# Performance work log

Hardware: AMD Instinct MI355X
Metric: run time of the kernel (lower is better)

## Reference

```python
import jax, jax.numpy as jnp
import numpy as np

B, S, D, H, W = 2, 2048, 1024, 16, 16  # batch, seq, embed, heads, window
HD = D // H
DFF = 4 * D
EPS = 1e-5


def _ln(x, g, b):
    m = jnp.mean(x, axis=-1, keepdims=True)
    v = jnp.mean(jnp.square(x - m), axis=-1, keepdims=True)
    return (x - m) * jax.lax.rsqrt(v + EPS) * g + b


def setup_inputs() -> dict:
    key = jax.random.key(0)
    ks = jax.random.split(key, 12)
    s = 0.02
    return {
        "x": jax.random.normal(ks[0], (B, S, D), jnp.float32),
        "ln1_g": jnp.ones((D,), jnp.float32),
        "ln1_b": jnp.zeros((D,), jnp.float32),
        "in_proj_w": jax.random.normal(ks[1], (3 * D, D), jnp.float32) * s,
        "in_proj_b": jnp.zeros((3 * D,), jnp.float32),
        "out_proj_w": jax.random.normal(ks[2], (D, D), jnp.float32) * s,
        "out_proj_b": jnp.zeros((D,), jnp.float32),
        "ln2_g": jnp.ones((D,), jnp.float32),
        "ln2_b": jnp.zeros((D,), jnp.float32),
        "mlp_w1": jax.random.normal(ks[3], (DFF, D), jnp.float32) * s,
        "mlp_b1": jnp.zeros((DFF,), jnp.float32),
        "mlp_w2": jax.random.normal(ks[4], (D, DFF), jnp.float32) * s,
        "mlp_b2": jnp.zeros((D,), jnp.float32),
    }


def reference(x, ln1_g, ln1_b, in_proj_w, in_proj_b, out_proj_w, out_proj_b,
              ln2_g, ln2_b, mlp_w1, mlp_b1, mlp_w2, mlp_b2):
    h = _ln(x, ln1_g, ln1_b)
    qkv = h @ in_proj_w.T + in_proj_b  # [B,S,3D]
    q, k, v = jnp.split(qkv, 3, axis=-1)
    q = q.reshape(B, S, H, HD)
    k = k.reshape(B, S, H, HD)
    v = v.reshape(B, S, H, HD)
    scores = jnp.einsum("bqhd,bkhd->bhqk", q, k) / jnp.sqrt(jnp.float32(HD))
    idx = jnp.arange(S)
    dlt = idx[:, None] - idx[None, :]
    allowed = (dlt >= 0) & (dlt < W)  # causal sliding window, width W
    scores = jnp.where(allowed, scores, -jnp.inf)
    attn = jax.nn.softmax(scores, axis=-1)
    o = jnp.einsum("bhqk,bkhd->bqhd", attn, v).reshape(B, S, D)
    o = o @ out_proj_w.T + out_proj_b
    x = x + o  # residual 1
    xn = _ln(x, ln2_g, ln2_b)
    mlp = jax.nn.gelu(xn @ mlp_w1.T + mlp_b1) @ mlp_w2.T + mlp_b2
    return x + mlp
```

## Files before the change

### kernel.cpp

```cpp
#include <hip/hip_runtime.h>
#include <hip/hip_bf16.h>
#include <cmath>

typedef __bf16 bf16;
typedef __bf16 bf16x4 __attribute__((ext_vector_type(4)));
typedef __bf16 bf16x8 __attribute__((ext_vector_type(8)));
typedef float f32x4 __attribute__((ext_vector_type(4)));

#define BB 2
#define SS 2048
#define DD 1024
#define HH 16
#define WW 16
#define HDD 64
#define DFFD 4096
#define NTOK (BB*SS)

__device__ __forceinline__ float gelu_f(float x) {
    const float k = 1.5957691216057308f;
    float u = k * (x + 0.044715f * x * x * x);
    return x / (1.0f + __expf(-u));
}

__device__ __forceinline__ void glds16(const bf16* g, const bf16* l) {
    __builtin_amdgcn_global_load_lds(
        (const __attribute__((address_space(1))) void*)(uintptr_t)(const void*)g,
        (__attribute__((address_space(3))) void*)(unsigned)(uintptr_t)(const void*)l,
        16, 0, 0);
}

__global__ __launch_bounds__(256) void conv_kernel(
    const float* __restrict__ src, bf16* __restrict__ dst, int n8)
{
    int i = blockIdx.x * 256 + threadIdx.x;
    if (i >= n8) return;
    f32x4 a = *(const f32x4*)(src + (size_t)i * 8);
    f32x4 b = *(const f32x4*)(src + (size_t)i * 8 + 4);
    bf16x8 v;
#pragma unroll
    for (int j = 0; j < 4; j++) { v[j] = (bf16)a[j]; v[4 + j] = (bf16)b[j]; }
    *(bf16x8*)(dst + (size_t)i * 8) = v;
}

__global__ __launch_bounds__(256) void ln_kernel(
    const float* __restrict__ x, const float* __restrict__ g, const float* __restrict__ b,
    bf16* __restrict__ out)
{
    const int row = blockIdx.x, t = threadIdx.x;
    f32x4 v = *(const f32x4*)(x + (size_t)row * DD + t * 4);
    float s  = v[0] + v[1] + v[2] + v[3];
    float s2 = v[0]*v[0] + v[1]*v[1] + v[2]*v[2] + v[3]*v[3];
#pragma unroll
    for (int off = 32; off >= 1; off >>= 1) {
        s  += __shfl_xor(s,  off, 64);
        s2 += __shfl_xor(s2, off, 64);
    }
    __shared__ float red[8];
    const int wave = t >> 6;
    if ((t & 63) == 0) { red[wave] = s; red[4 + wave] = s2; }
    __syncthreads();
    float ts  = red[0] + red[1] + red[2] + red[3];
    float ts2 = red[4] + red[5] + red[6] + red[7];
    float mean = ts * (1.0f / DD);
    float var  = ts2 * (1.0f / DD) - mean * mean;
    float rstd = rsqrtf(var + 1e-5f);
    f32x4 gv = *(const f32x4*)(g + t * 4);
    f32x4 bv = *(const f32x4*)(b + t * 4);
    bf16x4 o;
#pragma unroll
    for (int i = 0; i < 4; i++) o[i] = (bf16)((v[i] - mean) * rstd * gv[i] + bv[i]);
    *(bf16x4*)(out + (size_t)row * DD + t * 4) = o;
}

template<int TM, int ACT, int RESID, int OUTF32>
__global__ __launch_bounds__(256) void gemm_glds(
    const bf16* __restrict__ A, const bf16* __restrict__ Bw,
    const float* __restrict__ bias,
    const float* resid, void* __restrict__ Cout, int N, int K)
{
    constexpr int MI = 4;
    constexpr int NJ = (TM == 128) ? 4 : 2;
    __shared__ __align__(16) bf16 As[2 * TM * 32];
    __shared__ __align__(16) bf16 Bs[2 * 128 * 32];
    const int t = threadIdx.x;
    const int m0 = blockIdx.y * TM, n0 = blockIdx.x * 128;
    const int lane = t & 63, w = t >> 6;
    const int wm = (TM == 128) ? (w & 1) * 64 : 0;
    const int wn = (TM == 128) ? (w >> 1) * 64 : w * 32;
    const int quad = lane >> 4, l16 = lane & 15;
    const int srow = t >> 2, scol = (t & 3) * 8;

    const bf16* Ag = A  + (size_t)(m0 + srow) * K + scol;
    const bf16* Bg = Bw + (size_t)(n0 + srow) * K + scol;

    int k_lo = 0, k_hi = K;
    if (RESID == 3) {
        const int ks = K / gridDim.z;
        k_lo = blockIdx.z * ks;
        k_hi = k_lo + ks;
    }

    auto stage = [&](int buf, int k0) {
        const bf16* AsW = As + buf * (TM * 32) + w * 512;
        const bf16* BsW = Bs + buf * (128 * 32) + w * 512;
        glds16(Ag + k0, AsW);
        if (TM == 128) glds16(Ag + (size_t)64 * K + k0, AsW + 2048);
        glds16(Bg + k0, BsW);
        glds16(Bg + (size_t)64 * K + k0, BsW + 2048);
    };

    const f32x4 zero = {0.f, 0.f, 0.f, 0.f};
    f32x4 acc[MI][NJ];
#pragma unroll
    for (int i = 0; i < MI; i++)
#pragma unroll
        for (int j = 0; j < NJ; j++) acc[i][j] = zero;

    const int nsteps = (k_hi - k_lo) >> 5;
    stage(0, k_lo);
    __syncthreads();

    for (int step = 0; step < nsteps; ++step) {
        const int cur = step & 1;
        if (step + 1 < nsteps)
            stage(cur ^ 1, k_lo + ((step + 1) << 5));
        const bf16* Ab = As + cur * (TM * 32);
        const bf16* Bb = Bs + cur * (128 * 32);
        bf16x8 af[MI], bfr[NJ];
#pragma unroll
        for (int i = 0; i < MI; i++)
            af[i] = *(const bf16x8*)(Ab + (wm + i * 16 + l16) * 32 + quad * 8);
#pragma unroll
        for (int j = 0; j < NJ; j++)
            bfr[j] = *(const bf16x8*)(Bb + (wn + j * 16 + l16) * 32 + quad * 8);
#pragma unroll
        for (int i = 0; i < MI; i++)
#pragma unroll
            for (int j = 0; j < NJ; j++)
                acc[i][j] = __builtin_amdgcn_mfma_f32_16x16x32_bf16(af[i], bfr[j], acc[i][j], 0, 0, 0);
        __syncthreads();
    }

#pragma unroll
    for (int i = 0; i < MI; i++) {
#pragma unroll
        for (int j = 0; j < NJ; j++) {
            int col = n0 + wn + j * 16 + l16;
            float bv = bias[col];
            if (RESID == 3 && blockIdx.z != 0) bv = 0.0f;
#pragma unroll
            for (int r = 0; r < 4; r++) {
                int row = m0 + wm + i * 16 + quad * 4 + r;
                float val = acc[i][j][r] + bv;
                if (ACT == 1) val = gelu_f(val);
                size_t idx = (size_t)row * N + col;
                if (RESID == 2) val += resid[idx];
                if (RESID == 3) {
                    unsafeAtomicAdd(&((float*)Cout)[idx], val);
                } else if (OUTF32) {
                    ((float*)Cout)[idx] = val;
                } else {
                    ((bf16*)Cout)[idx] = (bf16)val;
                }
            }
        }
    }
}

__global__ __launch_bounds__(256) void attn_kernel(
    const bf16* __restrict__ qkv, bf16* __restrict__ o)
{
    __shared__ __align__(16) bf16 Vlds[4][32 * 64];
    __shared__ __align__(16) bf16 Plds[4][16 * 32];
    const int t = threadIdx.x;
    const int w = t >> 6, lane = t & 63;
    const int quad = lane >> 4, l16 = lane & 15;
    const int gw = blockIdx.x * 4 + w;
    const int qb = gw & 127;
    const int h  = (gw >> 7) & (HH - 1);
    const int b  = gw >> 11;
    const int q0 = qb << 4;
    const size_t rs = 3 * DD;
    const bf16* Qb = qkv + (size_t)b * SS * rs + h * HDD;
    const bf16* Kb = Qb + DD;
    const bf16* Vb = Qb + 2 * DD;
    bf16* Vw = Vlds[w];
    bf16* Pw = Plds[w];

    {
        const int sub = lane >> 3;
        const int dc  = (lane & 7) * 8;
#pragma unroll
        for (int c = 0; c < 4; c++) {
            int key = q0 - 16 + c * 8 + sub;
            if (key < 0) key = 0;
            glds16(Vb + (size_t)key * rs + dc, Vw + c * 512);
        }
    }

    const int qrow = q0 + l16;
    int kr0 = q0 - 16 + l16; if (kr0 < 0) kr0 = 0;
    bf16x8 qf0  = *(const bf16x8*)(Qb + (size_t)qrow * rs + quad * 8);
    bf16x8 qf1  = *(const bf16x8*)(Qb + (size_t)qrow * rs + 32 + quad * 8);
    bf16x8 kf0a = *(const bf16x8*)(Kb + (size_t)kr0  * rs + quad * 8);
    bf16x8 kf0b = *(const bf16x8*)(Kb + (size_t)kr0  * rs + 32 + quad * 8);
    bf16x8 kf1a = *(const bf16x8*)(Kb + (size_t)qrow * rs + quad * 8);
    bf16x8 kf1b = *(const bf16x8*)(Kb + (size_t)qrow * rs + 32 + quad * 8);

    const f32x4 zero = {0.f, 0.f, 0.f, 0.f};
    f32x4 acc0 = __builtin_amdgcn_mfma_f32_16x16x32_bf16(qf0, kf0a, zero, 0, 0, 0);
    acc0 = __builtin_amdgcn_mfma_f32_16x16x32_bf16(qf1, kf0b, acc0, 0, 0, 0);
    f32x4 acc1 = __builtin_amdgcn_mfma_f32_16x16x32_bf16(qf0, kf1a, zero, 0, 0, 0);
    acc1 = __builtin_amdgcn_mfma_f32_16x16x32_bf16(qf1, kf1b, acc1, 0, 0, 0);

    float rl[4];
#pragma unroll
    for (int r = 0; r < 4; r++) {
        const int row = quad * 4 + r;
        float s0 = (l16 > row && q0 - 16 + l16 >= 0) ? acc0[r] * 0.125f : -1e30f;
        float s1 = (l16 <= row)                      ? acc1[r] * 0.125f : -1e30f;
        float m = fmaxf(s0, s1);
        m = fmaxf(m, __shfl_xor(m, 1, 64));
        m = fmaxf(m, __shfl_xor(m, 2, 64));
        m = fmaxf(m, __shfl_xor(m, 4, 64));
        m = fmaxf(m, __shfl_xor(m, 8, 64));
        float e0 = __expf(s0 - m), e1 = __expf(s1 - m);
        float sum = e0 + e1;
        sum += __shfl_xor(sum, 1, 64);
        sum += __shfl_xor(sum, 2, 64);
        sum += __shfl_xor(sum, 4, 64);
        sum += __shfl_xor(sum, 8, 64);
        rl[r] = 1.0f / sum;
        Pw[row * 32 + l16]      = (bf16)e0;
        Pw[row * 32 + 16 + l16] = (bf16)e1;
    }

    asm volatile("s_waitcnt vmcnt(0)" ::: "memory");
    bf16x8 pf = *(const bf16x8*)(Pw + l16 * 32 + quad * 8);
#pragma unroll
    for (int dt = 0; dt < 4; dt++) {
        bf16x8 vf;
#pragma unroll
        for (int jj = 0; jj < 8; jj++)
            vf[jj] = Vw[(quad * 8 + jj) * 64 + dt * 16 + l16];
        f32x4 ov = __builtin_amdgcn_mfma_f32_16x16x32_bf16(pf, vf, zero, 0, 0, 0);
#pragma unroll
        for (int r = 0; r < 4; r++) {
            const int row = quad * 4 + r;
            o[(size_t)(b * SS + q0 + row) * DD + h * HDD + dt * 16 + l16] =
                (bf16)(ov[r] * rl[r]);
        }
    }
}

extern "C" void kernel_launch(void* const* d_in, const int* in_sizes, int n_in,
                              void* d_out, int out_size, void* d_ws, size_t ws_size,
                              hipStream_t stream)
{
    (void)in_sizes; (void)n_in; (void)out_size; (void)ws_size;
    const float* x    = (const float*)d_in[0];
    const float* ln1g = (const float*)d_in[1];
    const float* ln1b = (const float*)d_in[2];
    const float* Wqkv = (const float*)d_in[3];
    const float* bqkv = (const float*)d_in[4];
    const float* Wout = (const float*)d_in[5];
    const float* bout = (const float*)d_in[6];
    const float* ln2g = (const float*)d_in[7];
    const float* ln2b = (const float*)d_in[8];
    const float* W1   = (const float*)d_in[9];
    const float* b1   = (const float*)d_in[10];
    const float* W2   = (const float*)d_in[11];
    const float* b2   = (const float*)d_in[12];

    const size_t MB = (size_t)1 << 20;
    char* ws = (char*)d_ws;
    bf16* wqkv_bf = (bf16*)(ws);
    bf16* wout_bf = (bf16*)(ws + 6 * MB);
    bf16* w1_bf   = (bf16*)(ws);
    bf16* w2_bf   = (bf16*)(ws + 8 * MB);
    bf16* qkv     = (bf16*)(ws + 16 * MB);
    bf16* h1      = (bf16*)(ws + 16 * MB);
    bf16* hbuf    = (bf16*)(ws + 48 * MB);
    float* x1     = (float*)d_out;

    const dim3 blk(256);

    conv_kernel<<<(3 * DD * DD / 8) / 256, blk, 0, stream>>>(Wqkv, wqkv_bf, 3 * DD * DD / 8);
    conv_kernel<<<(DD * DD / 8) / 256, blk, 0, stream>>>(Wout, wout_bf, DD * DD / 8);
    ln_kernel<<<NTOK, blk, 0, stream>>>(x, ln1g, ln1b, hbuf);
    gemm_glds<128, 0, 0, 0><<<dim3(24, 32), blk, 0, stream>>>(
        hbuf, wqkv_bf, bqkv, nullptr, qkv, 3 * DD, DD);
    attn_kernel<<<BB * HH * (SS / 16) / 4, blk, 0, stream>>>(qkv, hbuf);
    gemm_glds<64, 0, 2, 1><<<dim3(8, 64), blk, 0, stream>>>(
        hbuf, wout_bf, bout, x, x1, DD, DD);

    conv_kernel<<<(DFFD * DD / 8) / 256, blk, 0, stream>>>(W1, w1_bf, DFFD * DD / 8);
    conv_kernel<<<(DFFD * DD / 8) / 256, blk, 0, stream>>>(W2, w2_bf, DFFD * DD / 8);
    ln_kernel<<<NTOK, blk, 0, stream>>>(x1, ln2g, ln2b, hbuf);
    gemm_glds<128, 1, 0, 0><<<dim3(32, 32), blk, 0, stream>>>(
        hbuf, w1_bf, b1, nullptr, h1, DFFD, DD);
    gemm_glds<128, 0, 3, 1><<<dim3(8, 32, 2), blk, 0, stream>>>(
        h1, w2_bf, b2, nullptr, x1, DD, DFFD);
}
```

Baseline: 316.2 us.

## Add 256x256 eight-wave GEMM with 4-deep LDS ring pipeline for QKV and MLP

Introduces a new GEMM kernel with 512 threads and 256x256 output tiles. It uses a four-stage LDS ring buffer filled by direct global-to-LDS loads, with explicit vmcnt waits and XOR swizzling to avoid bank conflicts, plus block-index swizzling and MFMA priority hints. The QKV, MLP1 and split-K MLP2 GEMMs move to it, and MLP2 now uses 4-way split-K with atomics. The aim is more data reuse per tile and better overlap of loads with MFMA work, at the cost of fewer blocks (low occupancy and wave-quantisation risk) and more atomic traffic.

```diff
diff --git a/kernel.cpp b/kernel.cpp
--- a/kernel.cpp
+++ b/kernel.cpp
@@ -72,6 +72,133 @@
     *(bf16x4*)(out + (size_t)row * DD + t * 4) = o;
 }
 
+template<int ACT, int RESID, int OUTF32>
+__global__ __launch_bounds__(512, 2) void gemm_8p(
+    const bf16* __restrict__ A, const bf16* __restrict__ Bw,
+    const float* __restrict__ bias,
+    void* __restrict__ Cout, int N, int K)
+{
+    __shared__ __align__(16) bf16 ring[4][16384];
+    const int t512 = threadIdx.x;
+    const int lane = t512 & 63, w = t512 >> 6;
+    const int quad = lane >> 4, l16 = lane & 15;
+    const int wm = (w >> 2) * 128;
+    const int wn = (w & 3) * 64;
+
+    const int nb  = gridDim.x * gridDim.y;
+    const int bid = blockIdx.y * gridDim.x + blockIdx.x;
+    const int cpx = nb >> 3;
+    const int swz = (bid & 7) * cpx + (bid >> 3);
+    const int m0 = (swz / gridDim.x) * 256;
+    const int n0 = (swz % gridDim.x) * 256;
+
+    int k_lo = 0, k_hi = K;
+    if (RESID == 3) { const int ks = K / gridDim.z; k_lo = blockIdx.z * ks; k_hi = k_lo + ks; }
+    const int NK = (k_hi - k_lo) >> 5;
+
+    const int srow = t512 >> 2;
+    auto stageA = [&](int u) {
+        const int k0 = k_lo + (u << 5);
+        const bf16* dst = ring[u & 3] + w * 512;
+#pragma unroll
+        for (int ra = 0; ra < 2; ra++) {
+            const int row = ra * 128 + srow;
+            const int q = (t512 & 3) ^ (row & 3);
+            glds16(A + (size_t)(m0 + row) * K + k0 + q * 8, dst + ra * 4096);
+        }
+    };
+    auto stageB = [&](int u) {
+        const int k0 = k_lo + (u << 5);
+        const bf16* dst = ring[u & 3] + 8192 + w * 512;
+#pragma unroll
+        for (int ra = 0; ra < 2; ra++) {
+            const int row = ra * 128 + srow;
+            const int q = (t512 & 3) ^ (row & 3);
+            glds16(Bw + (size_t)(n0 + row) * K + k0 + q * 8, dst + ra * 4096);
+        }
+    };
+
+    const f32x4 zero = {0.f, 0.f, 0.f, 0.f};
+    f32x4 acc[8][4];
+#pragma unroll
+    for (int i = 0; i < 8; i++)
+#pragma unroll
+        for (int j = 0; j < 4; j++) acc[i][j] = zero;
+
+    for (int u = 0; u < 3 && u < NK; ++u) { stageA(u); stageB(u); }
+
+    const int aswz = (l16 & 3);
+    for (int t = 0; t < NK; ++t) {
+        if (t < NK - 2)       asm volatile("s_waitcnt vmcnt(8)" ::: "memory");
+        else if (t == NK - 2) asm volatile("s_waitcnt vmcnt(4)" ::: "memory");
+        else                  asm volatile("s_waitcnt vmcnt(0)" ::: "memory");
+        __builtin_amdgcn_s_barrier();
+        const bf16* Ab = ring[t & 3];
+        const bf16* Bb = Ab + 8192;
+        bf16x8 af[4], bfr[4];
+#pragma unroll
+        for (int i = 0; i < 4; i++) {
+            const int row = wm + i * 16 + l16;
+            af[i] = *(const bf16x8*)(Ab + row * 32 + ((quad ^ aswz) * 8));
+        }
+#pragma unroll
+        for (int j = 0; j < 4; j++) {
+            const int row = wn + j * 16 + l16;
+            bfr[j] = *(const bf16x8*)(Bb + row * 32 + ((quad ^ aswz) * 8));
+        }
+        if (t + 3 < NK) stageA(t + 3);
+        asm volatile("s_waitcnt lgkmcnt(0)" ::: "memory");
+        __builtin_amdgcn_sched_barrier(0);
+        __builtin_amdgcn_s_setprio(1);
+#pragma unroll
+        for (int i = 0; i < 4; i++)
+#pragma unroll
+            for (int j = 0; j < 4; j++)
+                acc[i][j] = __builtin_amdgcn_mfma_f32_16x16x32_bf16(af[i], bfr[j], acc[i][j], 0, 0, 0);
+        __builtin_amdgcn_s_setprio(0);
+        __builtin_amdgcn_s_barrier();
+#pragma unroll
+        for (int i = 0; i < 4; i++) {
+            const int row = wm + 64 + i * 16 + l16;
+            af[i] = *(const bf16x8*)(Ab + row * 32 + ((quad ^ aswz) * 8));
+        }
+        if (t + 3 < NK) stageB(t + 3);
+        asm volatile("s_waitcnt lgkmcnt(0)" ::: "memory");
+        __builtin_amdgcn_sched_barrier(0);
+        __builtin_amdgcn_s_setprio(1);
+#pragma unroll
+        for (int i = 0; i < 4; i++)
+#pragma unroll
+            for (int j = 0; j < 4; j++)
+                acc[4 + i][j] = __builtin_amdgcn_mfma_f32_16x16x32_bf16(af[i], bfr[j], acc[4 + i][j], 0, 0, 0);
+        __builtin_amdgcn_s_setprio(0);
+    }
+
+#pragma unroll
+    for (int i = 0; i < 8; i++) {
+#pragma unroll
+        for (int j = 0; j < 4; j++) {
+            const int col = n0 + wn + j * 16 + l16;
+            float bv = bias[col];
+            if (RESID == 3 && blockIdx.z != 0) bv = 0.0f;
+#pragma unroll
+            for (int r = 0; r < 4; r++) {
+                const int row = m0 + wm + i * 16 + quad * 4 + r;
+                float val = acc[i][j][r] + bv;
+                if (ACT == 1) val = gelu_f(val);
+                size_t idx = (size_t)row * N + col;
+                if (RESID == 3) {
+                    unsafeAtomicAdd(&((float*)Cout)[idx], val);
+                } else if (OUTF32) {
+                    ((float*)Cout)[idx] = val;
+                } else {
+                    ((bf16*)Cout)[idx] = (bf16)val;
+                }
+            }
+        }
+    }
+}
+
 template<int TM, int ACT, int RESID, int OUTF32>
 __global__ __launch_bounds__(256) void gemm_glds(
     const bf16* __restrict__ A, const bf16* __restrict__ Bw,
@@ -93,13 +220,6 @@
     const bf16* Ag = A  + (size_t)(m0 + srow) * K + scol;
     const bf16* Bg = Bw + (size_t)(n0 + srow) * K + scol;
 
-    int k_lo = 0, k_hi = K;
-    if (RESID == 3) {
-        const int ks = K / gridDim.z;
-        k_lo = blockIdx.z * ks;
-        k_hi = k_lo + ks;
-    }
-
     auto stage = [&](int buf, int k0) {
         const bf16* AsW = As + buf * (TM * 32) + w * 512;
         const bf16* BsW = Bs + buf * (128 * 32) + w * 512;
@@ -116,14 +236,14 @@
 #pragma unroll
         for (int j = 0; j < NJ; j++) acc[i][j] = zero;
 
-    const int nsteps = (k_hi - k_lo) >> 5;
-    stage(0, k_lo);
+    const int nsteps = K >> 5;
+    stage(0, 0);
     __syncthreads();
 
     for (int step = 0; step < nsteps; ++step) {
         const int cur = step & 1;
         if (step + 1 < nsteps)
-            stage(cur ^ 1, k_lo + ((step + 1) << 5));
+            stage(cur ^ 1, (step + 1) << 5);
         const bf16* Ab = As + cur * (TM * 32);
         const bf16* Bb = Bs + cur * (128 * 32);
         bf16x8 af[MI], bfr[NJ];
@@ -147,7 +267,6 @@
         for (int j = 0; j < NJ; j++) {
             int col = n0 + wn + j * 16 + l16;
             float bv = bias[col];
-            if (RESID == 3 && blockIdx.z != 0) bv = 0.0f;
 #pragma unroll
             for (int r = 0; r < 4; r++) {
                 int row = m0 + wm + i * 16 + quad * 4 + r;
@@ -155,13 +274,8 @@
                 if (ACT == 1) val = gelu_f(val);
                 size_t idx = (size_t)row * N + col;
                 if (RESID == 2) val += resid[idx];
-                if (RESID == 3) {
-                    unsafeAtomicAdd(&((float*)Cout)[idx], val);
-                } else if (OUTF32) {
-                    ((float*)Cout)[idx] = val;
-                } else {
-                    ((bf16*)Cout)[idx] = (bf16)val;
-                }
+                if (OUTF32) ((float*)Cout)[idx] = val;
+                else        ((bf16*)Cout)[idx] = (bf16)val;
             }
         }
     }
@@ -284,12 +398,13 @@
     float* x1     = (float*)d_out;
 
     const dim3 blk(256);
+    const dim3 blk512(512);
 
     conv_kernel<<<(3 * DD * DD / 8) / 256, blk, 0, stream>>>(Wqkv, wqkv_bf, 3 * DD * DD / 8);
     conv_kernel<<<(DD * DD / 8) / 256, blk, 0, stream>>>(Wout, wout_bf, DD * DD / 8);
     ln_kernel<<<NTOK, blk, 0, stream>>>(x, ln1g, ln1b, hbuf);
-    gemm_glds<128, 0, 0, 0><<<dim3(24, 32), blk, 0, stream>>>(
-        hbuf, wqkv_bf, bqkv, nullptr, qkv, 3 * DD, DD);
+    gemm_8p<0, 0, 0><<<dim3(12, 16), blk512, 0, stream>>>(
+        hbuf, wqkv_bf, bqkv, qkv, 3 * DD, DD);
     attn_kernel<<<BB * HH * (SS / 16) / 4, blk, 0, stream>>>(qkv, hbuf);
     gemm_glds<64, 0, 2, 1><<<dim3(8, 64), blk, 0, stream>>>(
         hbuf, wout_bf, bout, x, x1, DD, DD);
@@ -297,8 +412,8 @@
     conv_kernel<<<(DFFD * DD / 8) / 256, blk, 0, stream>>>(W1, w1_bf, DFFD * DD / 8);
     conv_kernel<<<(DFFD * DD / 8) / 256, blk, 0, stream>>>(W2, w2_bf, DFFD * DD / 8);
     ln_kernel<<<NTOK, blk, 0, stream>>>(x1, ln2g, ln2b, hbuf);
-    gemm_glds<128, 1, 0, 0><<<dim3(32, 32), blk, 0, stream>>>(
-        hbuf, w1_bf, b1, nullptr, h1, DFFD, DD);
-    gemm_glds<128, 0, 3, 1><<<dim3(8, 32, 2), blk, 0, stream>>>(
-        h1, w2_bf, b2, nullptr, x1, DD, DFFD);
-}
+    gemm_8p<1, 0, 0><<<dim3(16, 16), blk512, 0, stream>>>(
+        hbuf, w1_bf, b1, h1, DFFD, DD);
+    gemm_8p<0, 3, 1><<<dim3(4, 16, 4), blk512, 0, stream>>>(
+        h1, w2_bf, b2, x1, DD, DFFD);
+}
```

Measured after the change: 318.0 us. About the same (+0.6%).

## Triple-buffer GEMM LDS staging with swizzled layout and one barrier per step

Applied to the files above, without the earlier changes.

The GEMM moves from double to triple buffering of the A/B tiles in shared memory. Two stages are in flight, gated by explicit vmcnt waits, and a single barrier per k-step replaces the two __syncthreads. The 16-byte chunk column is also XOR-swizzled by row on both the global-to-LDS copy and the fragment reads, to cut LDS bank conflicts. The cost is 50% more shared memory per block, which may lower occupancy, plus hand-coded waitcnt counts that must match the number of loads issued per stage.

```diff
diff --git a/kernel.cpp b/kernel.cpp
--- a/kernel.cpp
+++ b/kernel.cpp
@@ -80,18 +80,19 @@
 {
     constexpr int MI = 4;
     constexpr int NJ = (TM == 128) ? 4 : 2;
-    __shared__ __align__(16) bf16 As[2 * TM * 32];
-    __shared__ __align__(16) bf16 Bs[2 * 128 * 32];
+    __shared__ __align__(16) bf16 As[3 * TM * 32];
+    __shared__ __align__(16) bf16 Bs[3 * 128 * 32];
     const int t = threadIdx.x;
     const int m0 = blockIdx.y * TM, n0 = blockIdx.x * 128;
     const int lane = t & 63, w = t >> 6;
     const int wm = (TM == 128) ? (w & 1) * 64 : 0;
     const int wn = (TM == 128) ? (w >> 1) * 64 : w * 32;
     const int quad = lane >> 4, l16 = lane & 15;
-    const int srow = t >> 2, scol = (t & 3) * 8;
-
-    const bf16* Ag = A  + (size_t)(m0 + srow) * K + scol;
-    const bf16* Bg = Bw + (size_t)(n0 + srow) * K + scol;
+    const int srow = t >> 2;
+    const int qsw  = (t & 3) ^ ((srow >> 1) & 3);
+
+    const bf16* Ag = A  + (size_t)(m0 + srow) * K + qsw * 8;
+    const bf16* Bg = Bw + (size_t)(n0 + srow) * K + qsw * 8;
 
     int k_lo = 0, k_hi = K;
     if (RESID == 3) {
@@ -118,27 +119,37 @@
 
     const int nsteps = (k_hi - k_lo) >> 5;
     stage(0, k_lo);
-    __syncthreads();
-
+    if (nsteps > 1) stage(1, k_lo + 32);
+
+    const int rsl = (quad ^ ((l16 >> 1) & 3)) * 8;
+    int cur = 0, nxt2 = 2;
     for (int step = 0; step < nsteps; ++step) {
-        const int cur = step & 1;
-        if (step + 1 < nsteps)
-            stage(cur ^ 1, k_lo + ((step + 1) << 5));
+        if (step < nsteps - 1) {
+            if (TM == 128) asm volatile("s_waitcnt vmcnt(4)" ::: "memory");
+            else           asm volatile("s_waitcnt vmcnt(3)" ::: "memory");
+        } else {
+            asm volatile("s_waitcnt vmcnt(0)" ::: "memory");
+        }
+        __builtin_amdgcn_s_barrier();
         const bf16* Ab = As + cur * (TM * 32);
         const bf16* Bb = Bs + cur * (128 * 32);
         bf16x8 af[MI], bfr[NJ];
 #pragma unroll
         for (int i = 0; i < MI; i++)
-            af[i] = *(const bf16x8*)(Ab + (wm + i * 16 + l16) * 32 + quad * 8);
+            af[i] = *(const bf16x8*)(Ab + (wm + i * 16 + l16) * 32 + rsl);
 #pragma unroll
         for (int j = 0; j < NJ; j++)
-            bfr[j] = *(const bf16x8*)(Bb + (wn + j * 16 + l16) * 32 + quad * 8);
+            bfr[j] = *(const bf16x8*)(Bb + (wn + j * 16 + l16) * 32 + rsl);
+        if (step + 2 < nsteps) stage(nxt2, k_lo + ((step + 2) << 5));
+        asm volatile("s_waitcnt lgkmcnt(0)" ::: "memory");
+        __builtin_amdgcn_sched_barrier(0);
 #pragma unroll
         for (int i = 0; i < MI; i++)
 #pragma unroll
             for (int j = 0; j < NJ; j++)
                 acc[i][j] = __builtin_amdgcn_mfma_f32_16x16x32_bf16(af[i], bfr[j], acc[i][j], 0, 0, 0);
-        __syncthreads();
+        cur  = (cur  + 1 == 3) ? 0 : cur  + 1;
+        nxt2 = (nxt2 + 1 == 3) ? 0 : nxt2 + 1;
     }
 
 #pragma unroll
```

Result: faster. 302.1 us (-4.4%).
